# Performance work log

Hardware: AMD Instinct MI355X
Metric: run time of the kernel (lower is better)

## Reference

```python
import jax, jax.numpy as jnp
import numpy as np

G = 4096   # num_genes
P = 4096   # num_perts
H = 64     # hidden_size
B = 4      # num_graphs
E1 = 81920 # coexpress edges
E2 = 81920 # GO edges
FF = 512   # transformer ffn
NH = 2     # attention heads
INTER, LAT = 32, 16  # VAE dims

def _bn(x, g, b, eps=1e-5):
    # BatchNorm1d in training mode: batch stats (biased var)
    m = x.mean(0); v = x.var(0)
    return (x - m) / jnp.sqrt(v + eps) * g + b

def _ln(x, g, b, eps=1e-5):
    m = x.mean(-1, keepdims=True); v = x.var(-1, keepdims=True)
    return (x - m) / jnp.sqrt(v + eps) * g + b

def _mlp2(x, w1, b1, g1, be1, w2, b2, g2, be2):
    # MLP([a,b,c]) builds Linear->BN->ReLU->Linear->BN (trailing ReLU stripped)
    h = jax.nn.relu(_bn(x @ w1.T + b1, g1, be1))
    return _bn(h @ w2.T + b2, g2, be2)

def _sgconv(x, ei, ew, w, b, n):
    # SGConv K=1: gcn_norm (self loops, symmetric norm) then linear
    src = jnp.concatenate([ei[0], jnp.arange(n)])
    dst = jnp.concatenate([ei[1], jnp.arange(n)])
    wgt = jnp.concatenate([ew, jnp.ones((n,), ew.dtype)])
    deg = jax.ops.segment_sum(wgt, dst, num_segments=n)
    dinv = jnp.where(deg > 0, 1.0 / jnp.sqrt(jnp.where(deg > 0, deg, 1.0)), 0.0)
    norm = dinv[dst] * wgt * dinv[src]
    agg = jax.ops.segment_sum(norm[:, None] * x[src], dst, num_segments=n)
    return agg @ w.T + b

def setup_inputs():
    ks = iter(jax.random.split(jax.random.key(0), 80))
    def nrm(shape, s=0.05):
        return jax.random.normal(next(ks), shape, dtype=jnp.float32) * s
    d = {}
    d['x'] = jax.random.uniform(next(ks), (B * G,), dtype=jnp.float32)
    d['pert_idx'] = jax.random.randint(next(ks), (B, 2), 0, P)
    d['mask'] = jnp.zeros((G, G), jnp.float32)
    d['ei_co'] = jax.random.randint(next(ks), (2, E1), 0, G)
    d['w_co'] = jax.random.uniform(next(ks), (E1,), dtype=jnp.float32)
    d['ei_go'] = jax.random.randint(next(ks), (2, E2), 0, P)
    d['w_go'] = jax.random.uniform(next(ks), (E2,), dtype=jnp.float32)
    d['gene_emb'] = nrm((G, H)); d['emb_pos'] = nrm((G, H)); d['pert_tbl'] = nrm((P, H))
    d['sg_co_w'] = nrm((H, H)); d['sg_co_b'] = jnp.zeros((H,))
    d['sg_go_w'] = nrm((H, H)); d['sg_go_b'] = jnp.zeros((H,))
    d['bn_emb_g'] = jnp.ones((H,)); d['bn_emb_b'] = jnp.zeros((H,))
    for pre, din, dout in [('etv2_1', H, H), ('etv2_2', H, H), ('pf_1', H, H), ('pf_2', H, H), ('rw_1', H, 2 * H), ('rw_2', 2 * H, H)]:
        d[pre + '_w'] = nrm((dout, din)); d[pre + '_b'] = jnp.zeros((dout,))
        d[pre + '_g'] = jnp.ones((dout,)); d[pre + '_be'] = jnp.zeros((dout,))
    d['bnpb_g'] = jnp.ones((H,)); d['bnpb_b'] = jnp.zeros((H,))
    d['attn_in_w'] = nrm((3 * H, H)); d['attn_in_b'] = jnp.zeros((3 * H,))
    d['attn_out_w'] = nrm((H, H)); d['attn_out_b'] = jnp.zeros((H,))
    d['ln1_g'] = jnp.ones((H,)); d['ln1_b'] = jnp.zeros((H,))
    d['ff1_w'] = nrm((FF, H)); d['ff1_b'] = jnp.zeros((FF,))
    d['ff2_w'] = nrm((H, FF)); d['ff2_b'] = jnp.zeros((H,))
    d['ln2_g'] = jnp.ones((H,)); d['ln2_b'] = jnp.zeros((H,))
    d['indv_w1'] = nrm((G, H)); d['indv_b1'] = jnp.zeros((G,))
    d['vae_e1_w'] = nrm((INTER, G)); d['vae_e1_b'] = jnp.zeros((INTER,))
    d['vae_mu_w'] = nrm((LAT, INTER)); d['vae_mu_b'] = jnp.zeros((LAT,))
    d['vae_lv_w'] = nrm((LAT, INTER)); d['vae_lv_b'] = jnp.zeros((LAT,))
    d['vae_d1_w'] = nrm((INTER, LAT)); d['vae_d1_b'] = jnp.zeros((INTER,))
    d['vae_d2_w'] = nrm((G, INTER)); d['vae_d2_b'] = jnp.zeros((G,))
    d['eps'] = jax.random.normal(next(ks), (B, LAT), dtype=jnp.float32)
    return d

def reference(x, pert_idx, mask, ei_co, w_co, ei_go, w_go, gene_emb, emb_pos, pert_tbl, sg_co_w, sg_co_b, sg_go_w, sg_go_b, bn_emb_g, bn_emb_b, etv2_1_w, etv2_1_b, etv2_1_g, etv2_1_be, etv2_2_w, etv2_2_b, etv2_2_g, etv2_2_be, pf_1_w, pf_1_b, pf_1_g, pf_1_be, pf_2_w, pf_2_b, pf_2_g, pf_2_be, rw_1_w, rw_1_b, rw_1_g, rw_1_be, rw_2_w, rw_2_b, rw_2_g, rw_2_be, bnpb_g, bnpb_b, attn_in_w, attn_in_b, attn_out_w, attn_out_b, ln1_g, ln1_b, ff1_w, ff1_b, ff2_w, ff2_b, ln2_g, ln2_b, indv_w1, indv_b1, vae_e1_w, vae_e1_b, vae_mu_w, vae_mu_b, vae_lv_w, vae_lv_b, vae_d1_w, vae_d1_b, vae_d2_w, vae_d2_b, eps):
    # gene base embedding (identical across graphs until pert fusion)
    base = jax.nn.relu(_bn(gene_emb, bn_emb_g, bn_emb_b))               # [G,H]
    pos = _sgconv(emb_pos, ei_co, w_co, sg_co_w, sg_co_b, G)            # 1 gene-GNN layer
    base = base + 0.2 * pos
    base = _mlp2(base, etv2_1_w, etv2_1_b, etv2_1_g, etv2_1_be, etv2_2_w, etv2_2_b, etv2_2_g, etv2_2_be)
    # pert embeddings propagated on GO graph
    pge = _sgconv(pert_tbl, ei_go, w_go, sg_go_w, sg_go_b, P)           # [P,H]
    # per-graph pert_track: sum of pert embeddings (all pert_idx valid)
    psum = pge[pert_idx].sum(axis=1)                                    # [B,H]
    etot = _mlp2(psum, pf_1_w, pf_1_b, pf_1_g, pf_1_be, pf_2_w, pf_2_b, pf_2_g, pf_2_be)
    base_b = base[None, :, :] + etot[:, None, :]                        # [B,G,H]
    flat = jax.nn.relu(_bn(base_b.reshape(B * G, H), bnpb_g, bnpb_b))
    out = _mlp2(flat, rw_1_w, rw_1_b, rw_1_g, rw_1_be, rw_2_w, rw_2_b, rw_2_g, rw_2_be)
    out = out.reshape(B, G, H)
    # transformer encoder layer (post-norm, relu, nhead=2), eval/no-dropout
    qkv = out @ attn_in_w.T + attn_in_b
    q, k, v = jnp.split(qkv, 3, axis=-1)
    hd = H // NH
    q = q.reshape(B, G, NH, hd); k = k.reshape(B, G, NH, hd); v = v.reshape(B, G, NH, hd)
    sc = jnp.einsum('bqhd,bkhd->bhqk', q, k) / np.float32(np.sqrt(hd)) + mask
    a = jax.nn.softmax(sc, axis=-1)
    ctx = jnp.einsum('bhqk,bkhd->bqhd', a, v).reshape(B, G, H)
    att = ctx @ attn_out_w.T + attn_out_b
    h1 = _ln(out + att, ln1_g, ln1_b)
    ff = jax.nn.relu(h1 @ ff1_w.T + ff1_b) @ ff2_w.T + ff2_b
    enc = _ln(h1 + ff, ln2_g, ln2_b)
    # per-gene linear: (enc.unsqueeze(-1)*indv_w1).sum(2)+indv_b1
    pred0 = jnp.einsum('bgh,gh->bg', enc, indv_w1) + indv_b1
    # VAE branch on raw expression
    xr = x.reshape(B, G)
    he = jax.nn.relu(xr @ vae_e1_w.T + vae_e1_b)
    mu = he @ vae_mu_w.T + vae_mu_b
    lv = he @ vae_lv_w.T + vae_lv_b
    z = mu + eps * jnp.exp(0.5 * lv)
    hdc = jax.nn.relu(z @ vae_d1_w.T + vae_d1_b)
    recon = hdc @ vae_d2_w.T + vae_d2_b
    kl = -0.5 * jnp.mean(jnp.sum(1.0 + lv - mu ** 2 - jnp.exp(lv), axis=1))
    recon = jnp.where(xr == 0, 0.0, recon)
    pred = pred0 + recon
    return (pred, kl)
```

## Files before the change

### kernel.cpp

```cpp
#include <hip/hip_runtime.h>
#include <hip/hip_bf16.h>
#include <math.h>

#define GG 4096
#define PP 4096
#define HH 64
#define BB 4
#define E1N 81920
#define E2N 81920
#define FFD 512
#define BNEPS 1e-5f
#define LOG2E 1.44269504088896341f
#define QPRE (0.17677669529663687f * LOG2E)

typedef unsigned short ushort_t;
typedef unsigned int uint_t;
using sh8 = __attribute__((ext_vector_type(8))) short;
using sh4 = __attribute__((ext_vector_type(4))) short;
using f4  = __attribute__((ext_vector_type(4))) float;

struct MaskOn  { static constexpr bool v = true; };
struct MaskOff { static constexpr bool v = false; };

#if __has_builtin(__builtin_amdgcn_mfma_f32_16x16x16bf16_1k)
// ... 341 lines not shown
        dev_pert_edges(bid - 320, pidx, ei_go, w_go, ws + OF_DEGGO, pert_tbl, ws + OF_PSLOT);
    else dev_vae_mid(ws + OF_HE, vmu_w, vmu_b, vlv_w, vlv_b, vd1_w, vd1_b, veps,
                     ws + OF_HDC, klout, sh);
}

__global__ void k_fat4(float* ws, const float* __restrict__ gene_emb,
                       const float* __restrict__ emb_pos,
                       const float* __restrict__ sg_co_w, const float* __restrict__ sg_co_b,
                       const float* __restrict__ bn_emb_g, const float* __restrict__ bn_emb_b,
                       const int* __restrict__ pidx, const float* __restrict__ pert_tbl,
                       const float* __restrict__ gw, const float* __restrict__ gb,
                       const float* __restrict__ w1, const float* __restrict__ b1,
                       const float* __restrict__ g1, const float* __restrict__ be1,
                       const float* __restrict__ w2, const float* __restrict__ b2,
                       const float* __restrict__ g2, const float* __restrict__ be2) {
    __shared__ float sh[4416];
    int bid = blockIdx.x;
    if (bid < 1024)
        dev_base_combine(bid, gene_emb, (const int*)(ws + OF_OFFS),
                         (const int*)(ws + OF_SSRC), ws + OF_SNRM,
                         emb_pos, ws + OF_DEGCO,
                         sg_co_w, sg_co_b, ws + OF_STATS, ws + OF_STATS + 128,
                         bn_emb_g, bn_emb_b, ws + OF_BASEIN, sh);
    else
        dev_pert_mlp(ws + OF_PSLOT, pidx, ws + OF_DEGGO, pert_tbl, gw, gb,
                     w1, b1, g1, be1, w2, b2, g2, be2, ws + OF_ETOT, sh);
}

__launch_bounds__(256)
__global__ void k_gemm64(const float* __restrict__ X, const float* __restrict__ W,
                         const float* __restrict__ bias, float* __restrict__ Y,
                         int Cin, int Cout,
                         const float* __restrict__ bnsum, const float* __restrict__ bnsq,
                         const float* __restrict__ bng, const float* __restrict__ bnb,
                         float invN, int relu_in,
                         float* __restrict__ outsum, float* __restrict__ outsq) {
    __shared__ float Xs[64][66];
    __shared__ float Ws[64][66];
    __shared__ float bsc[64], bsh[64];
    const int t = threadIdx.x;
    const int row0 = blockIdx.x * 64, cb = blockIdx.y * 64;
    const int tx = t & 15, ty = t >> 4;
    const int c0 = tx * 4, r0 = ty * 4;
    float acc[4][4];
    #pragma unroll
    for (int j = 0; j < 4; j++)
        #pragma unroll
        for (int i = 0; i < 4; i++) acc[j][i] = 0.f;

    for (int k0 = 0; k0 < Cin; k0 += 64) {
        __syncthreads();
        if (t < 64) {
            float sc = 1.f, sh = 0.f;
            if (bnsum) {
                int c = k0 + t;
                float m = bnsum[c] * invN;
                float is_ = rsqrtf(bnsq[c] * invN - m * m + BNEPS);
                sc = is_ * bng[c]; sh = bnb[c] - m * sc;
            }
            bsc[t] = sc; bsh[t] = sh;
        }
        __syncthreads();
        for (int i = t; i < 1024; i += 256) {
            int r = i >> 4, kq = (i & 15) * 4;
            float4 v = *(const float4*)&X[(size_t)(row0 + r) * Cin + k0 + kq];
            float e0 = v.x * bsc[kq] + bsh[kq];
            float e1 = v.y * bsc[kq + 1] + bsh[kq + 1];
            float e2 = v.z * bsc[kq + 2] + bsh[kq + 2];
            float e3 = v.w * bsc[kq + 3] + bsh[kq + 3];
            if (relu_in) {
                e0 = fmaxf(e0, 0.f); e1 = fmaxf(e1, 0.f);
                e2 = fmaxf(e2, 0.f); e3 = fmaxf(e3, 0.f);
            }
            Xs[r][kq] = e0; Xs[r][kq + 1] = e1; Xs[r][kq + 2] = e2; Xs[r][kq + 3] = e3;
            float4 wv = *(const float4*)&W[(size_t)(cb + r) * Cin + k0 + kq];
            Ws[r][kq] = wv.x; Ws[r][kq + 1] = wv.y; Ws[r][kq + 2] = wv.z; Ws[r][kq + 3] = wv.w;
        }
        __syncthreads();
        #pragma unroll 4
        for (int k = 0; k < 64; k += 2) {
            float2 a[4], b[4];
            #pragma unroll
            for (int j = 0; j < 4; j++) a[j] = *(const float2*)&Xs[r0 + j][k];
            #pragma unroll
            for (int i = 0; i < 4; i++) b[i] = *(const float2*)&Ws[c0 + i][k];
            #pragma unroll
            for (int j = 0; j < 4; j++)
                #pragma unroll
                for (int i = 0; i < 4; i++)
                    acc[j][i] += a[j].x * b[i].x + a[j].y * b[i].y;
        }
    }
    float4 bi = *(const float4*)&bias[cb + c0];
    float scol[4] = {0.f, 0.f, 0.f, 0.f}, qcol[4] = {0.f, 0.f, 0.f, 0.f};
    #pragma unroll
    for (int j = 0; j < 4; j++) {
        float4 o;
        o.x = acc[j][0] + bi.x; o.y = acc[j][1] + bi.y;
        o.z = acc[j][2] + bi.z; o.w = acc[j][3] + bi.w;
        *(float4*)&Y[(size_t)(row0 + r0 + j) * Cout + cb + c0] = o;
        scol[0] += o.x; scol[1] += o.y; scol[2] += o.z; scol[3] += o.w;
        qcol[0] += o.x * o.x; qcol[1] += o.y * o.y;
        qcol[2] += o.z * o.z; qcol[3] += o.w * o.w;
    }
    if (outsum) {
        __syncthreads();
        #pragma unroll
        for (int i = 0; i < 4; i++) { Xs[ty][c0 + i] = scol[i]; Ws[ty][c0 + i] = qcol[i]; }
        __syncthreads();
        if (t < 64) {
            float ss = 0.f, qq = 0.f;
            #pragma unroll
            for (int r = 0; r < 16; r++) { ss += Xs[r][t]; qq += Ws[r][t]; }
            atomicAdd(&outsum[cb + t], ss);
            atomicAdd(&outsq[cb + t], qq);
        }
    }
}

__launch_bounds__(256)
__global__ void k_gemm_rw1(const float* __restrict__ y2, const float* __restrict__ etot,
                           const float* __restrict__ s2sum, const float* __restrict__ s2sq,
                           const float* __restrict__ g2e, const float* __restrict__ b2e,
                           const float* __restrict__ g3, const float* __restrict__ b3,
                           const float* __restrict__ W, const float* __restrict__ bias,
                           float* __restrict__ Y,
                           float* __restrict__ osum, float* __restrict__ osq) {
    __shared__ float Xs[64][66];
    __shared__ float Ws[64][66];
    __shared__ float bsc[64], bsh[64];
    const int t = threadIdx.x;
    const int row0 = blockIdx.x * 64, cb = blockIdx.y * 64;
    const int tx = t & 15, ty = t >> 4;
    const int c0 = tx * 4, r0 = ty * 4;
    const int bb = row0 >> 12;
    if (t < 64) {
        const float iG = 1.0f / 4096.f, iNG = 1.0f / 16384.f;
        float S1 = s2sum[t], S2 = s2sq[t];
        float m2 = S1 * iG;
        float is2 = rsqrtf(S2 * iG - m2 * m2 + BNEPS);
        float sc2 = is2 * g2e[t], sh2 = b2e[t] - m2 * sc2;
        float sz = sc2 * S1 + 4096.f * sh2;
        float szz = sc2 * sc2 * S2 + 2.f * sc2 * sh2 * S1 + 4096.f * sh2 * sh2;
        float e0 = etot[t], e1 = etot[64 + t], e2 = etot[128 + t], e3 = etot[192 + t];
        float se = e0 + e1 + e2 + e3;
        float see = e0 * e0 + e1 * e1 + e2 * e2 + e3 * e3;
        float sumF = 4.f * sz + 4096.f * se;
        float sqF = 4.f * szz + 2.f * sz * se + 4096.f * see;
        float m3 = sumF * iNG;
        float is3 = rsqrtf(sqF * iNG - m3 * m3 + BNEPS);
        float eb = etot[bb * 64 + t];
        bsc[t] = sc2 * is3 * g3[t];
        bsh[t] = (sh2 + eb - m3) * is3 * g3[t] + b3[t];
    }
    __syncthreads();
    for (int i = t; i < 1024; i += 256) {
        int r = i >> 4, kq = (i & 15) * 4;
        int g = (row0 + r) & 4095;
        float4 v = *(const float4*)&y2[(size_t)g * 64 + kq];
        Xs[r][kq] = fmaxf(v.x * bsc[kq] + bsh[kq], 0.f);
        Xs[r][kq + 1] = fmaxf(v.y * bsc[kq + 1] + bsh[kq + 1], 0.f);
        Xs[r][kq + 2] = fmaxf(v.z * bsc[kq + 2] + bsh[kq + 2], 0.f);
        Xs[r][kq + 3] = fmaxf(v.w * bsc[kq + 3] + bsh[kq + 3], 0.f);
        float4 wv = *(const float4*)&W[(size_t)(cb + r) * 64 + kq];
        Ws[r][kq] = wv.x; Ws[r][kq + 1] = wv.y; Ws[r][kq + 2] = wv.z; Ws[r][kq + 3] = wv.w;
    }
    __syncthreads();
    float acc[4][4];
    #pragma unroll
    for (int j = 0; j < 4; j++)
        #pragma unroll
        for (int i = 0; i < 4; i++) acc[j][i] = 0.f;
    #pragma unroll 4
    for (int k = 0; k < 64; k += 2) {
        float2 a[4], b[4];
        #pragma unroll
        for (int j = 0; j < 4; j++) a[j] = *(const float2*)&Xs[r0 + j][k];
        #pragma unroll
        for (int i = 0; i < 4; i++) b[i] = *(const float2*)&Ws[c0 + i][k];
        #pragma unroll
        for (int j = 0; j < 4; j++)
            #pragma unroll
            for (int i = 0; i < 4; i++)
                acc[j][i] += a[j].x * b[i].x + a[j].y * b[i].y;
    }
    float4 bi = *(const float4*)&bias[cb + c0];
    float scol[4] = {0.f, 0.f, 0.f, 0.f}, qcol[4] = {0.f, 0.f, 0.f, 0.f};
    #pragma unroll
    for (int j = 0; j < 4; j++) {
        float4 o;
        o.x = acc[j][0] + bi.x; o.y = acc[j][1] + bi.y;
        o.z = acc[j][2] + bi.z; o.w = acc[j][3] + bi.w;
        *(float4*)&Y[(size_t)(row0 + r0 + j) * 128 + cb + c0] = o;
        scol[0] += o.x; scol[1] += o.y; scol[2] += o.z; scol[3] += o.w;
        qcol[0] += o.x * o.x; qcol[1] += o.y * o.y;
        qcol[2] += o.z * o.z; qcol[3] += o.w * o.w;
    }
    __syncthreads();
    #pragma unroll
    for (int i = 0; i < 4; i++) { Xs[ty][c0 + i] = scol[i]; Ws[ty][c0 + i] = qcol[i]; }
    __syncthreads();
    if (t < 64) {
        float ss = 0.f, qq = 0.f;
        #pragma unroll
        for (int r = 0; r < 16; r++) { ss += Xs[r][t]; qq += Ws[r][t]; }
        atomicAdd(&osum[cb + t], ss);
        atomicAdd(&osq[cb + t], qq);
    }
}

__launch_bounds__(256)
__global__ void k_gemm_qkv(const float* __restrict__ X, const float* __restrict__ W,
                           const float* __restrict__ bias,
                           const float* __restrict__ bnsum, const float* __restrict__ bnsq,
                           const float* __restrict__ bng, const float* __restrict__ bnb,
                           ushort_t* __restrict__ Qb, ushort_t* __restrict__ Kb,
                           ushort_t* __restrict__ Vf) {
    __shared__ float Xs[64][66];
    __shared__ float Ws[64][66];
    __shared__ float bsc[64], bsh[64];
    const int t = threadIdx.x;
    const int row0 = blockIdx.x * 64, yb = blockIdx.y, cb = yb * 64;
    const int tx = t & 15, ty = t >> 4;
    const int c0 = tx * 4, r0 = ty * 4;
    const float invN = 1.0f / (float)(BB * GG);
    if (t < 64) {
        float m = bnsum[t] * invN;
        float is_ = rsqrtf(bnsq[t] * invN - m * m + BNEPS);
        float sc = is_ * bng[t];
        bsc[t] = sc; bsh[t] = bnb[t] - m * sc;
    }
    __syncthreads();
    for (int i = t; i < 1024; i += 256) {
        int r = i >> 4, kq = (i & 15) * 4;
        float4 v = *(const float4*)&X[(size_t)(row0 + r) * 64 + kq];
        Xs[r][kq] = v.x * bsc[kq] + bsh[kq];
        Xs[r][kq + 1] = v.y * bsc[kq + 1] + bsh[kq + 1];
        Xs[r][kq + 2] = v.z * bsc[kq + 2] + bsh[kq + 2];
        Xs[r][kq + 3] = v.w * bsc[kq + 3] + bsh[kq + 3];
        float4 wv = *(const float4*)&W[(size_t)(cb + r) * 64 + kq];
        Ws[r][kq] = wv.x; Ws[r][kq + 1] = wv.y; Ws[r][kq + 2] = wv.z; Ws[r][kq + 3] = wv.w;
    }
    __syncthreads();
    float acc[4][4];
    #pragma unroll
    for (int j = 0; j < 4; j++)
        #pragma unroll
        for (int i = 0; i < 4; i++) acc[j][i] = 0.f;
    #pragma unroll 4
    for (int k = 0; k < 64; k += 2) {
        float2 a[4], b[4];
        #pragma unroll
        for (int j = 0; j < 4; j++) a[j] = *(const float2*)&Xs[r0 + j][k];
        #pragma unroll
        for (int i = 0; i < 4; i++) b[i] = *(const float2*)&Ws[c0 + i][k];
        #pragma unroll
        for (int j = 0; j < 4; j++)
            #pragma unroll
            for (int i = 0; i < 4; i++)
                acc[j][i] += a[j].x * b[i].x + a[j].y * b[i].y;
    }
    float4 bi = *(const float4*)&bias[cb + c0];
    const int b2 = row0 >> 12, tile = (row0 & 4095) >> 6;
    if (yb < 2) {
        ushort_t* Dst = (yb == 0) ? Qb : Kb;
        const float sc2 = (yb == 0) ? QPRE : 1.0f;
        const int h = c0 >> 5, d = c0 & 31;
        #pragma unroll
        for (int j = 0; j < 4; j++) {
            union { ushort_t u[4]; uint2 v; } pk;
            pk.u[0] = f2b((acc[j][0] + bi.x) * sc2);
            pk.u[1] = f2b((acc[j][1] + bi.y) * sc2);
            pk.u[2] = f2b((acc[j][2] + bi.z) * sc2);
            pk.u[3] = f2b((acc[j][3] + bi.w) * sc2);
            int g = (row0 & 4095) + r0 + j;
            *(uint2*)&Dst[((size_t)(b2 * 2 + h) * GG + g) * 32 + d] = pk.v;
        }
    } else {
        __syncthreads();
        #pragma unroll
        for (int j = 0; j < 4; j++) {
            Xs[r0 + j][c0] = acc[j][0] + bi.x;
            Xs[r0 + j][c0 + 1] = acc[j][1] + bi.y;
            Xs[r0 + j][c0 + 2] = acc[j][2] + bi.z;
            Xs[r0 + j][c0 + 3] = acc[j][3] + bi.w;
        }
        __syncthreads();
        #pragma unroll
        for (int h = 0; h < 2; h++) {
            union { ushort_t u[8]; uint4 v; } pk;
            #pragma unroll
            for (int j = 0; j < 8; j++) {
                int idx = t * 8 + j;
                int g2 = idx >> 8, L = (idx >> 2) & 63, i = idx & 3;
                int key = (g2 >> 1) * 16 + ((L >> 4) << 2) + i;
                int d = ((g2 & 1) << 4) + (L & 15);
                pk.u[j] = f2b(Xs[key][h * 32 + d]);
            }
            *(uint4*)&Vf[((size_t)((b2 * 2 + h) * 64 + tile)) * 2048 + t * 8] = pk.v;
        }
    }
}

__launch_bounds__(512, 8)
__global__ void k_attn_mfma(const ushort_t* __restrict__ Qb, const ushort_t* __restrict__ Kb,
                            const ushort_t* __restrict__ Vf, const float* __restrict__ mask,
                            const float* __restrict__ mflag,
                            float* __restrict__ opA, float* __restrict__ opB,
                            float* __restrict__ Lp) {
    __shared__ ushort_t Kl[2][2][2048];
    __shared__ ushort_t Vl[2][2][2048];
    const int split = blockIdx.y;
    const int bh0 = blockIdx.z * 2;
    const int q0 = blockIdx.x * 64;
    const int kstart = split * (GG / 4), kend = kstart + (GG / 4);
    const int t = threadIdx.x;
    const int lane = t & 63, w = t >> 6;
    const int qg = w >> 1, kh = w & 1;
    const int l15 = lane & 15, quad = lane >> 4;
    const int i2a = kh * 2, i2b = kh * 2 + 1;
    const int um = (*(const int*)mflag) != 0;

    sh8 qf[2];
    #pragma unroll
    for (int bh = 0; bh < 2; bh++)
        qf[bh] = *(const sh8*)&Qb[((size_t)(bh0 + bh) * GG + q0 + qg * 16 + l15) * 32 + quad * 8];
    const float* mrow = mask + (size_t)(q0 + qg * 16 + l15) * GG + quad * 4;

    auto stage = [&](int buf, int k0) {
        int bh = t >> 8, c = t & 255;
        int key = ((c >> 6) << 4) + (c & 15);
        int chunk = (c >> 4) & 3;
        gld16(Kb + ((size_t)(bh0 + bh) * GG + k0 + key) * 32 + chunk * 8,
              &Kl[buf][bh][c * 8]);
        gld16(Vf + ((size_t)((bh0 + bh) * 64 + (k0 >> 6))) * 2048 + c * 8,
              &Vl[buf][bh][c * 8]);
    };
    stage(0, kstart);

    f4 O0[2], O1[2];
    float ls[2];
    #pragma unroll
    for (int bh = 0; bh < 2; bh++) {
        O0[bh] = f4{0.f, 0.f, 0.f, 0.f};
        O1[bh] = f4{0.f, 0.f, 0.f, 0.f};
        ls[bh] = 0.f;
    }

    auto run = [&](auto tag) {
        constexpr bool U = decltype(tag)::v;
        const float4 zf4 = {0.f, 0.f, 0.f, 0.f};
        float4 mva = zf4, mvb = zf4;
        if constexpr (U) {
            mva = *(const float4*)&mrow[kstart + i2a * 16];
            mvb = *(const float4*)&mrow[kstart + i2b * 16];
        }
        for (int k0 = kstart; k0 < kend; k0 += 64) {
            const int cur = ((k0 - kstart) >> 6) & 1;
            __syncthreads();
            if (k0 + 64 < kend) stage(cur ^ 1, k0 + 64);
            float4 mva_n = zf4, mvb_n = zf4;
            if constexpr (U) {
                const int kp = (k0 + 64 < kend) ? (k0 + 64) : k0;
                mva_n = *(const float4*)&mrow[kp + i2a * 16];
                mvb_n = *(const float4*)&mrow[kp + i2b * 16];
            }
            #pragma unroll
            for (int bh = 0; bh < 2; bh++) {
                sh8 kfa = *(const sh8*)&Kl[cur][bh][(i2a * 64 + lane) * 8];
                sh8 kfb = *(const sh8*)&Kl[cur][bh][(i2b * 64 + lane) * 8];
                f4 z = {0.f, 0.f, 0.f, 0.f};
                f4 sa = __builtin_amdgcn_mfma_f32_16x16x32_bf16(kfa, qf[bh], z, 0, 0, 0);
                f4 sb = __builtin_amdgcn_mfma_f32_16x16x32_bf16(kfb, qf[bh], z, 0, 0, 0);
                {
                    float p0, p1, p2, p3;
                    if constexpr (U) {
                        p0 = exp2f(fmaf(mva.x, LOG2E, sa[0]));
                        p1 = exp2f(fmaf(mva.y, LOG2E, sa[1]));
                        p2 = exp2f(fmaf(mva.z, LOG2E, sa[2]));
                        p3 = exp2f(fmaf(mva.w, LOG2E, sa[3]));
                    } else {
                        p0 = exp2f(sa[0]); p1 = exp2f(sa[1]);
                        p2 = exp2f(sa[2]); p3 = exp2f(sa[3]);
                    }
                    ls[bh] += (p0 + p1) + (p2 + p3);
                    union { __hip_bfloat162 h2[2]; sh4 v; } pkp;
                    pkp.h2[0] = __float22bfloat162_rn(float2{p0, p1});
                    pkp.h2[1] = __float22bfloat162_rn(float2{p2, p3});
                    sh4 vf0 = *(const sh4*)&Vl[cur][bh][((i2a * 2 + 0) * 64 + lane) * 4];
                    sh4 vf1 = *(const sh4*)&Vl[cur][bh][((i2a * 2 + 1) * 64 + lane) * 4];
                    O0[bh] = MFMA16(pkp.v, vf0, O0[bh]);
                    O1[bh] = MFMA16(pkp.v, vf1, O1[bh]);
                }
                {
                    float p0, p1, p2, p3;
                    if constexpr (U) {
                        p0 = exp2f(fmaf(mvb.x, LOG2E, sb[0]));
                        p1 = exp2f(fmaf(mvb.y, LOG2E, sb[1]));
                        p2 = exp2f(fmaf(mvb.z, LOG2E, sb[2]));
                        p3 = exp2f(fmaf(mvb.w, LOG2E, sb[3]));
                    } else {
                        p0 = exp2f(sb[0]); p1 = exp2f(sb[1]);
                        p2 = exp2f(sb[2]); p3 = exp2f(sb[3]);
                    }
                    ls[bh] += (p0 + p1) + (p2 + p3);
                    union { __hip_bfloat162 h2[2]; sh4 v; } pkp;
                    pkp.h2[0] = __float22bfloat162_rn(float2{p0, p1});
                    pkp.h2[1] = __float22bfloat162_rn(float2{p2, p3});
                    sh4 vf0 = *(const sh4*)&Vl[cur][bh][((i2b * 2 + 0) * 64 + lane) * 4];
                    sh4 vf1 = *(const sh4*)&Vl[cur][bh][((i2b * 2 + 1) * 64 + lane) * 4];
                    O0[bh] = MFMA16(pkp.v, vf0, O0[bh]);
                    O1[bh] = MFMA16(pkp.v, vf1, O1[bh]);
                }
            }
            if constexpr (U) { mva = mva_n; mvb = mvb_n; }
        }
    };
    if (um) run(MaskOn{}); else run(MaskOff{});

    #pragma unroll
    for (int bh = 0; bh < 2; bh++) {
        ls[bh] += __shfl_xor(ls[bh], 16, 64);
        ls[bh] += __shfl_xor(ls[bh], 32, 64);
    }
    __syncthreads();
    float* Ox = (float*)&Kl[0][0][0];
    float* Lx = (float*)&Vl[0][0][0];
    if (kh == 0) {
        #pragma unroll
        for (int bh = 0; bh < 2; bh++) {
            #pragma unroll
            for (int r = 0; r < 4; r++) {
                int ql = qg * 16 + quad * 4 + r;
                Ox[(bh * 64 + ql) * 32 + l15] = O0[bh][r];
                Ox[(bh * 64 + ql) * 32 + l15 + 16] = O1[bh][r];
            }
            if (quad == 0) Lx[bh * 64 + qg * 16 + l15] = ls[bh];
        }
    }
    __syncthreads();
    if (kh == 1) {
        float* op = (split < 3) ? (opA + (size_t)split * OPS) : opB;
        #pragma unroll
        for (int bh = 0; bh < 2; bh++) {
            int gbh = bh0 + bh;
            #pragma unroll
            for (int r = 0; r < 4; r++) {
                int ql = qg * 16 + quad * 4 + r;
                size_t o = ((size_t)gbh * GG + q0 + ql) * 32 + l15;
                op[o] = O0[bh][r] + Ox[(bh * 64 + ql) * 32 + l15];
                op[o + 16] = O1[bh][r] + Ox[(bh * 64 + ql) * 32 + l15 + 16];
            }
            if (quad == 0)
                Lp[split * 32768 + gbh * GG + q0 + qg * 16 + l15] =
                    ls[bh] + Lx[bh * 64 + qg * 16 + l15];
        }
    }
}

__launch_bounds__(256)
__global__ void k_tail(const float* __restrict__ opA, const float* __restrict__ opB,
                       const float* __restrict__ Lp, const float* __restrict__ yrw2,
                       const float* __restrict__ Waout, const float* __restrict__ baout,
                       const float* __restrict__ bsum5, const float* __restrict__ bsq5,
                       const float* __restrict__ bg5, const float* __restrict__ bb5,
                       const float* __restrict__ lg1, const float* __restrict__ lb1,
                       const ushort_t* __restrict__ W1b, const float* __restrict__ b1f,
                       const ushort_t* __restrict__ W2b, const float* __restrict__ b2f,
                       const float* __restrict__ lg2, const float* __restrict__ lb2,
                       const float* __restrict__ indvw, const float* __restrict__ indvb,
                       const float* __restrict__ hdc, const float* __restrict__ d2w,
                       const float* __restrict__ d2b, const float* __restrict__ x,
                       float* __restrict__ outp) {
    __shared__ float Wt[4160];
    __shared__ float Cs[4160];
    __shared__ ushort_t Hb[4096];
    __shared__ ushort_t FT[32768];
    __shared__ ushort_t WS[2][4096];
    const int t = threadIdx.x;
    const int r0b = blockIdx.x * 64;
    const int lane = t & 63, w = t >> 6;
    const int l15 = lane & 15, quad = lane >> 4;

    for (int i = t; i < 4096; i += 256) Wt[(i & 63) * 65 + (i >> 6)] = Waout[i];
    {
        int col = t & 63, rl = t >> 6;
        int hh = col >> 5, d = col & 31;
        for (int jj = 0; jj < 16; jj++) {
            int lrow = rl + jj * 4;
            int row = r0b + lrow;
            int b = row >> 12, q = row & 4095;
            int bhq = (b * 2 + hh) * GG + q;
            size_t oi = (size_t)bhq * 32 + d;
            float num = opA[oi] + opA[OPS + oi] + opA[2 * OPS + oi] + opB[oi];
            float den = Lp[bhq] + Lp[32768 + bhq] + Lp[65536 + bhq] + Lp[98304 + bhq];
            Cs[lrow * 65 + col] = num / den;
        }
    }
    __syncthreads();
    const float invN = 1.0f / (float)(BB * GG);
    float m5 = bsum5[lane] * invN;
    float is5 = rsqrtf(bsq5[lane] * invN - m5 * m5 + BNEPS);
    float h1v[16];
    for (int j = 0; j < 16; j++) {
        int lrow = w * 16 + j;
        int row = r0b + lrow;
        float acc = baout[lane];
        const float* cr = Cs + lrow * 65;
        #pragma unroll 8
        for (int k = 0; k < 64; k++) acc += cr[k] * Wt[k * 65 + lane];
        float ov = (yrw2[(size_t)row * 64 + lane] - m5) * is5 * bg5[lane] + bb5[lane];
        float v = ov + acc;
        float s = v;
        for (int o = 32; o > 0; o >>= 1) s += __shfl_xor(s, o, 64);
        float mean = s * (1.f / 64.f);
        float d = v - mean;
        float sq = d * d;
        for (int o = 32; o > 0; o >>= 1) sq += __shfl_xor(sq, o, 64);
        float inv = rsqrtf(sq * (1.f / 64.f) + BNEPS);
        h1v[j] = d * inv * lg1[lane] + lb1[lane];
    }
    __syncthreads();
    float* h1f = Wt;
    for (int j = 0; j < 16; j++) h1f[(w * 16 + j) * 65 + lane] = h1v[j];
    __syncthreads();
    if (t < 128) {
        int kt = t >> 6, lane6 = t & 63;
        int q2 = (lane6 >> 4) & 3, r15 = lane6 & 15;
        for (int rg = 0; rg < 4; rg++) {
            union { ushort_t u[8]; uint4 v4; } pk;
            #pragma unroll
            for (int j = 0; j < 8; j++)
                pk.u[j] = f2b(h1f[(rg * 16 + r15) * 65 + kt * 32 + q2 * 8 + j]);
            *(uint4*)&Hb[(rg * 2 + kt) * 512 + lane6 * 8] = pk.v4;
        }
    }
    auto stage1 = [&](int buf, int cb8) {
        int cb = cb8 * 64;
        #pragma unroll
        for (int kt = 0; kt < 2; kt++)
            gld16(W1b + (size_t)((cb + w * 16 + l15) * 64 + kt * 32 + quad * 8),
                  &WS[buf][(w * 2 + kt) * 512 + lane * 8]);
    };
    stage1(0, 0);
    for (int cb8 = 0; cb8 < 8; cb8++) {
        const int cur = cb8 & 1;
        __syncthreads();
        if (cb8 + 1 < 8) stage1(cur ^ 1, cb8 + 1);
        sh8 xf0 = *(const sh8*)&Hb[(w * 2 + 0) * 512 + lane * 8];
        sh8 xf1 = *(const sh8*)&Hb[(w * 2 + 1) * 512 + lane * 8];
        const int cb = cb8 * 64;
        #pragma unroll
        for (int c = 0; c < 4; c++) {
            sh8 wf0 = *(const sh8*)&WS[cur][(c * 2 + 0) * 512 + lane * 8];
            sh8 wf1 = *(const sh8*)&WS[cur][(c * 2 + 1) * 512 + lane * 8];
            f4 z = {0.f, 0.f, 0.f, 0.f};
            f4 acc = __builtin_amdgcn_mfma_f32_16x16x32_bf16(wf0, xf0, z, 0, 0, 0);
            acc = __builtin_amdgcn_mfma_f32_16x16x32_bf16(wf1, xf1, acc, 0, 0, 0);
            float4 bv = *(const float4*)&b1f[cb + c * 16 + quad * 4];
            union { ushort_t u[4]; uint2 v2; } pk;
            pk.u[0] = f2b(fmaxf(acc[0] + bv.x, 0.f));
            pk.u[1] = f2b(fmaxf(acc[1] + bv.y, 0.f));
            pk.u[2] = f2b(fmaxf(acc[2] + bv.z, 0.f));
            pk.u[3] = f2b(fmaxf(acc[3] + bv.w, 0.f));
            int kt512 = cb8 * 2 + (c >> 1);
            int quadp = (c & 1) * 2 + (quad >> 1);
            int j0 = (quad & 1) * 4;
            *(uint2*)&FT[((w * 16 + kt512) * 64 + quadp * 16 + l15) * 8 + j0] = pk.v2;
        }
    }
    auto stage2 = [&](int buf, int k0) {
        #pragma unroll
        for (int kt = 0; kt < 2; kt++)
            gld16(W2b + (size_t)((w * 16 + l15) * 512 + k0 + kt * 32 + quad * 8),
                  &WS[buf][(w * 2 + kt) * 512 + lane * 8]);
    };
    stage2(0, 0);
    f4 acc2[4];
    #pragma unroll
    for (int c = 0; c < 4; c++) acc2[c] = f4{0.f, 0.f, 0.f, 0.f};
    for (int k0 = 0; k0 < 512; k0 += 64) {
        const int cur = (k0 >> 6) & 1;
        __syncthreads();
        if (k0 + 64 < 512) stage2(cur ^ 1, k0 + 64);
        const int ktb = k0 >> 5;
        #pragma unroll
        for (int kt = 0; kt < 2; kt++) {
            sh8 xf = *(const sh8*)&FT[((w * 16 + ktb + kt) * 64 + lane) * 8];
            #pragma unroll
            for (int c = 0; c < 4; c++) {
                sh8 wf = *(const sh8*)&WS[cur][(c * 2 + kt) * 512 + lane * 8];
                acc2[c] = __builtin_amdgcn_mfma_f32_16x16x32_bf16(wf, xf, acc2[c], 0, 0, 0);
            }
        }
    }
    const int row = r0b + w * 16 + l15;
    const int b = row >> 12, g = row & 4095;
    float v[4][4];
    float s = 0.f, sq = 0.f;
    #pragma unroll
    for (int c = 0; c < 4; c++) {
        float4 bv = *(const float4*)&b2f[c * 16 + quad * 4];
        #pragma unroll
        for (int i = 0; i < 4; i++) {
            float hv = h1f[(w * 16 + l15) * 65 + c * 16 + quad * 4 + i];
            float bvi = (i == 0) ? bv.x : (i == 1) ? bv.y : (i == 2) ? bv.z : bv.w;
            v[c][i] = hv + acc2[c][i] + bvi;
            s += v[c][i]; sq += v[c][i] * v[c][i];
        }
    }
    s += __shfl_xor(s, 16, 64);  s += __shfl_xor(s, 32, 64);
    sq += __shfl_xor(sq, 16, 64); sq += __shfl_xor(sq, 32, 64);
    float mean = s * (1.f / 64.f);
    float inv = rsqrtf(sq * (1.f / 64.f) - mean * mean + BNEPS);
    float pd = 0.f;
    #pragma unroll
    for (int c = 0; c < 4; c++) {
        float4 lgv = *(const float4*)&lg2[c * 16 + quad * 4];
        float4 lbv = *(const float4*)&lb2[c * 16 + quad * 4];
        float4 iwv = *(const float4*)&indvw[(size_t)g * 64 + c * 16 + quad * 4];
        pd += ((v[c][0] - mean) * inv * lgv.x + lbv.x) * iwv.x;
        pd += ((v[c][1] - mean) * inv * lgv.y + lbv.y) * iwv.y;
        pd += ((v[c][2] - mean) * inv * lgv.z + lbv.z) * iwv.z;
        pd += ((v[c][3] - mean) * inv * lgv.w + lbv.w) * iwv.w;
    }
    float rc = 0.f;
    #pragma unroll
    for (int i = 0; i < 8; i++)
        rc += hdc[b * 32 + quad * 8 + i] * d2w[(size_t)g * 32 + quad * 8 + i];
    pd += __shfl_xor(pd, 16, 64); pd += __shfl_xor(pd, 32, 64);
    rc += __shfl_xor(rc, 16, 64); rc += __shfl_xor(rc, 32, 64);
    if (quad == 0) {
        float recon = rc + d2b[g];
        if (x[row] == 0.f) recon = 0.f;
        outp[row] = pd + indvb[g] + recon;
    }
}

extern "C" void kernel_launch(void* const* d_in, const int* in_sizes, int n_in,
                              void* d_out, int out_size, void* d_ws, size_t ws_size,
                              hipStream_t stream) {
    const float* x        = (const float*)d_in[0];
    const int*   pert_idx = (const int*)  d_in[1];
    const float* mask     = (const float*)d_in[2];
    const int*   ei_co    = (const int*)  d_in[3];
    const float* w_co     = (const float*)d_in[4];
    const int*   ei_go    = (const int*)  d_in[5];
    const float* w_go     = (const float*)d_in[6];
    const float* gene_emb = (const float*)d_in[7];
    const float* emb_pos  = (const float*)d_in[8];
    const float* pert_tbl = (const float*)d_in[9];
    const float* sg_co_w  = (const float*)d_in[10];
    const float* sg_co_b  = (const float*)d_in[11];
    const float* sg_go_w  = (const float*)d_in[12];
    const float* sg_go_b  = (const float*)d_in[13];
    const float* bn_emb_g = (const float*)d_in[14];
    const float* bn_emb_b = (const float*)d_in[15];
    const float* etv1_w   = (const float*)d_in[16];
    const float* etv1_b   = (const float*)d_in[17];
    const float* etv1_g   = (const float*)d_in[18];
    const float* etv1_be  = (const float*)d_in[19];
    const float* etv2_w   = (const float*)d_in[20];
    const float* etv2_b   = (const float*)d_in[21];
    const float* etv2_g   = (const float*)d_in[22];
    const float* etv2_be  = (const float*)d_in[23];
    const float* pf1_w    = (const float*)d_in[24];
    const float* pf1_b    = (const float*)d_in[25];
    const float* pf1_g    = (const float*)d_in[26];
    const float* pf1_be   = (const float*)d_in[27];
    const float* pf2_w    = (const float*)d_in[28];
    const float* pf2_b    = (const float*)d_in[29];
    const float* pf2_g    = (const float*)d_in[30];
    const float* pf2_be   = (const float*)d_in[31];
    const float* rw1_w    = (const float*)d_in[32];
    const float* rw1_b    = (const float*)d_in[33];
    const float* rw1_g    = (const float*)d_in[34];
    const float* rw1_be   = (const float*)d_in[35];
    const float* rw2_w    = (const float*)d_in[36];
    const float* rw2_b    = (const float*)d_in[37];
    const float* rw2_g    = (const float*)d_in[38];
    const float* rw2_be   = (const float*)d_in[39];
    const float* bnpb_g   = (const float*)d_in[40];
    const float* bnpb_b   = (const float*)d_in[41];
    const float* ain_w    = (const float*)d_in[42];
    const float* ain_b    = (const float*)d_in[43];
    const float* aout_w   = (const float*)d_in[44];
    const float* aout_b   = (const float*)d_in[45];
    const float* ln1_g    = (const float*)d_in[46];
    const float* ln1_b    = (const float*)d_in[47];
    const float* ff1_w    = (const float*)d_in[48];
    const float* ff1_b    = (const float*)d_in[49];
    const float* ff2_w    = (const float*)d_in[50];
    const float* ff2_b    = (const float*)d_in[51];
    const float* ln2_g    = (const float*)d_in[52];
    const float* ln2_b    = (const float*)d_in[53];
    const float* indv_w   = (const float*)d_in[54];
    const float* indv_b   = (const float*)d_in[55];
    const float* ve1_w    = (const float*)d_in[56];
    const float* ve1_b    = (const float*)d_in[57];
    const float* vmu_w    = (const float*)d_in[58];
    const float* vmu_b    = (const float*)d_in[59];
    const float* vlv_w    = (const float*)d_in[60];
    const float* vlv_b    = (const float*)d_in[61];
    const float* vd1_w    = (const float*)d_in[62];
    const float* vd1_b    = (const float*)d_in[63];
    const float* vd2_w    = (const float*)d_in[64];
    const float* vd2_b    = (const float*)d_in[65];
    const float* veps     = (const float*)d_in[66];

    float* ws   = (float*)d_ws;
    float* outp = (float*)d_out;

    float* stm1 = ws + OF_STATS + 1 * 256; float* sti1 = stm1 + 128;
    float* stm2 = ws + OF_STATS + 2 * 256; float* sti2 = stm2 + 128;
    float* stm4 = ws + OF_STATS + 4 * 256; float* sti4 = stm4 + 128;
    float* stm5 = ws + OF_STATS + 5 * 256; float* sti5 = stm5 + 128;

    float* basein = ws + OF_BASEIN;
    float* y1     = ws + OF_Y1;
    float* y2     = ws + OF_Y2;
    float* yrw1   = ws + OF_RW1;
    float* yrw2   = ws + OF_RW2;
    float* opA    = ws + OF_OPA;
    float* opB    = ws + OF_OPB;
    float* Lp     = ws + OF_LP;
    ushort_t* Qb  = (ushort_t*)(ws + OF_QB);
    ushort_t* Kb  = (ushort_t*)(ws + OF_KB);
    ushort_t* Vf  = (ushort_t*)(ws + OF_VF);
    ushort_t* W1b = (ushort_t*)(ws + OF_W1B);
    ushort_t* W2b = (ushort_t*)(ws + OF_W2B);

    const int NG = BB * GG;
    const float iG = 1.0f / (float)GG, iNG = 1.0f / (float)NG;

    hipMemsetAsync(ws, 0, 11268 * sizeof(float), stream);
    hipMemsetAsync(ws + OF_CNT, 0, 4096 * sizeof(int), stream);

    k_fat12<<<1792, 256, 0, stream>>>(ws, ei_co, w_co, ei_go, w_go, gene_emb,
                                      x, ve1_w, ve1_b, ff1_w, ff2_w, mask);
    k_scan<<<1, 256, 0, stream>>>(ws);
    k_fat3<<<641, 256, 0, stream>>>(ws, ei_co, w_co, pert_idx,
                                    ei_go, w_go, pert_tbl,
                                    vmu_w, vmu_b, vlv_w, vlv_b, vd1_w, vd1_b,
                                    veps, outp + NG);
    k_fat4<<<1025, 256, 0, stream>>>(ws, gene_emb, emb_pos, sg_co_w, sg_co_b,
                                     bn_emb_g, bn_emb_b, pert_idx, pert_tbl,
                                     sg_go_w, sg_go_b,
                                     pf1_w, pf1_b, pf1_g, pf1_be,
                                     pf2_w, pf2_b, pf2_g, pf2_be);
    k_gemm64<<<dim3(GG / 64, 1), 256, 0, stream>>>(basein, etv1_w, etv1_b, y1, 64, 64,
                                                   nullptr, nullptr, nullptr, nullptr, 0.f, 0,
                                                   stm1, sti1);
    k_gemm64<<<dim3(GG / 64, 1), 256, 0, stream>>>(y1, etv2_w, etv2_b, y2, 64, 64,
                                                   stm1, sti1, etv1_g, etv1_be, iG, 1,
                                                   stm2, sti2);
    k_gemm_rw1<<<dim3(NG / 64, 2), 256, 0, stream>>>(y2, ws + OF_ETOT, stm2, sti2,
                                                     etv2_g, etv2_be, bnpb_g, bnpb_b,
                                                     rw1_w, rw1_b, yrw1, stm4, sti4);
    k_gemm64<<<dim3(NG / 64, 1), 256, 0, stream>>>(yrw1, rw2_w, rw2_b, yrw2, 128, 64,
                                                   stm4, sti4, rw1_g, rw1_be, iNG, 1,
                                                   stm5, sti5);
    k_gemm_qkv<<<dim3(NG / 64, 3), 256, 0, stream>>>(yrw2, ain_w, ain_b,
                                                     stm5, sti5, rw2_g, rw2_be,
                                                     Qb, Kb, Vf);
    k_attn_mfma<<<dim3(GG / 64, 4, 4), 512, 0, stream>>>(Qb, Kb, Vf, mask,
                                                         ws + OF_MFLAG, opA, opB, Lp);
    k_tail<<<NG / 64, 256, 0, stream>>>(opA, opB, Lp, yrw2, aout_w, aout_b,
                                        stm5, sti5, rw2_g, rw2_be, ln1_g, ln1_b,
                                        W1b, ff1_b, W2b, ff2_b, ln2_g, ln2_b,
                                        indv_w, indv_b, ws + OF_HDC, vd2_w, vd2_b,
                                        x, outp);
}
```

Before: 455.4 us.

## Halve attention key splits and double key tile per iteration

The attention kernel now splits the key range two ways instead of four, and each iteration stages and processes 128 keys instead of 64. Shared memory K/V buffers double and the launch bound drops to 4 blocks per CU. The split-combine in the tail kernel reads only two partial outputs and normalisers. The aim is to cut partial-sum traffic and the number of barriers per key. The cost is fewer blocks in flight (512 instead of 1024), lower occupancy, and mask loads that are no longer prefetched one iteration ahead.

```diff
diff --git a/kernel.cpp b/kernel.cpp
--- a/kernel.cpp
+++ b/kernel.cpp
@@ -667,23 +667,22 @@
     }
 }
 
-__launch_bounds__(512, 8)
+__launch_bounds__(512, 4)
 __global__ void k_attn_mfma(const ushort_t* __restrict__ Qb, const ushort_t* __restrict__ Kb,
                             const ushort_t* __restrict__ Vf, const float* __restrict__ mask,
                             const float* __restrict__ mflag,
                             float* __restrict__ opA, float* __restrict__ opB,
                             float* __restrict__ Lp) {
-    __shared__ ushort_t Kl[2][2][2048];
-    __shared__ ushort_t Vl[2][2][2048];
+    __shared__ ushort_t Kl[2][2][4096];
+    __shared__ ushort_t Vl[2][2][4096];
     const int split = blockIdx.y;
     const int bh0 = blockIdx.z * 2;
     const int q0 = blockIdx.x * 64;
-    const int kstart = split * (GG / 4), kend = kstart + (GG / 4);
+    const int kstart = split * (GG / 2), kend = kstart + (GG / 2);
     const int t = threadIdx.x;
     const int lane = t & 63, w = t >> 6;
     const int qg = w >> 1, kh = w & 1;
     const int l15 = lane & 15, quad = lane >> 4;
-    const int i2a = kh * 2, i2b = kh * 2 + 1;
     const int um = (*(const int*)mflag) != 0;
 
     sh8 qf[2];
@@ -696,10 +695,13 @@
         int bh = t >> 8, c = t & 255;
         int key = ((c >> 6) << 4) + (c & 15);
         int chunk = (c >> 4) & 3;
-        gld16(Kb + ((size_t)(bh0 + bh) * GG + k0 + key) * 32 + chunk * 8,
-              &Kl[buf][bh][c * 8]);
-        gld16(Vf + ((size_t)((bh0 + bh) * 64 + (k0 >> 6))) * 2048 + c * 8,
-              &Vl[buf][bh][c * 8]);
+        #pragma unroll
+        for (int s = 0; s < 2; s++) {
+            gld16(Kb + ((size_t)(bh0 + bh) * GG + k0 + s * 64 + key) * 32 + chunk * 8,
+                  &Kl[buf][bh][s * 2048 + c * 8]);
+            gld16(Vf + ((size_t)((bh0 + bh) * 64 + (k0 >> 6) + s)) * 2048 + c * 8,
+                  &Vl[buf][bh][s * 2048 + c * 8]);
+        }
     };
     stage(0, kstart);
 
@@ -714,36 +716,25 @@
 
     auto run = [&](auto tag) {
         constexpr bool U = decltype(tag)::v;
-        const float4 zf4 = {0.f, 0.f, 0.f, 0.f};
-        float4 mva = zf4, mvb = zf4;
-        if constexpr (U) {
-            mva = *(const float4*)&mrow[kstart + i2a * 16];
-            mvb = *(const float4*)&mrow[kstart + i2b * 16];
-        }
-        for (int k0 = kstart; k0 < kend; k0 += 64) {
-            const int cur = ((k0 - kstart) >> 6) & 1;
+        for (int k0 = kstart; k0 < kend; k0 += 128) {
+            const int cur = ((k0 - kstart) >> 7) & 1;
             __syncthreads();
-            if (k0 + 64 < kend) stage(cur ^ 1, k0 + 64);
-            float4 mva_n = zf4, mvb_n = zf4;
-            if constexpr (U) {
-                const int kp = (k0 + 64 < kend) ? (k0 + 64) : k0;
-                mva_n = *(const float4*)&mrow[kp + i2a * 16];
-                mvb_n = *(const float4*)&mrow[kp + i2b * 16];
-            }
+            if (k0 + 128 < kend) stage(cur ^ 1, k0 + 128);
             #pragma unroll
             for (int bh = 0; bh < 2; bh++) {
-                sh8 kfa = *(const sh8*)&Kl[cur][bh][(i2a * 64 + lane) * 8];
-                sh8 kfb = *(const sh8*)&Kl[cur][bh][(i2b * 64 + lane) * 8];
-                f4 z = {0.f, 0.f, 0.f, 0.f};
-                f4 sa = __builtin_amdgcn_mfma_f32_16x16x32_bf16(kfa, qf[bh], z, 0, 0, 0);
-                f4 sb = __builtin_amdgcn_mfma_f32_16x16x32_bf16(kfb, qf[bh], z, 0, 0, 0);
-                {
+                #pragma unroll
+                for (int ii = 0; ii < 4; ii++) {
+                    const int i2 = kh * 4 + ii;
+                    sh8 kf = *(const sh8*)&Kl[cur][bh][(i2 * 64 + lane) * 8];
+                    f4 z = {0.f, 0.f, 0.f, 0.f};
+                    f4 sa = __builtin_amdgcn_mfma_f32_16x16x32_bf16(kf, qf[bh], z, 0, 0, 0);
                     float p0, p1, p2, p3;
                     if constexpr (U) {
-                        p0 = exp2f(fmaf(mva.x, LOG2E, sa[0]));
-                        p1 = exp2f(fmaf(mva.y, LOG2E, sa[1]));
-                        p2 = exp2f(fmaf(mva.z, LOG2E, sa[2]));
-                        p3 = exp2f(fmaf(mva.w, LOG2E, sa[3]));
+                        float4 mv = *(const float4*)&mrow[k0 + i2 * 16];
+                        p0 = exp2f(fmaf(mv.x, LOG2E, sa[0]));
+                        p1 = exp2f(fmaf(mv.y, LOG2E, sa[1]));
+                        p2 = exp2f(fmaf(mv.z, LOG2E, sa[2]));
+                        p3 = exp2f(fmaf(mv.w, LOG2E, sa[3]));
                     } else {
                         p0 = exp2f(sa[0]); p1 = exp2f(sa[1]);
                         p2 = exp2f(sa[2]); p3 = exp2f(sa[3]);
@@ -752,33 +743,12 @@
                     union { __hip_bfloat162 h2[2]; sh4 v; } pkp;
                     pkp.h2[0] = __float22bfloat162_rn(float2{p0, p1});
                     pkp.h2[1] = __float22bfloat162_rn(float2{p2, p3});
-                    sh4 vf0 = *(const sh4*)&Vl[cur][bh][((i2a * 2 + 0) * 64 + lane) * 4];
-                    sh4 vf1 = *(const sh4*)&Vl[cur][bh][((i2a * 2 + 1) * 64 + lane) * 4];
-                    O0[bh] = MFMA16(pkp.v, vf0, O0[bh]);
-                    O1[bh] = MFMA16(pkp.v, vf1, O1[bh]);
-                }
-                {
-                    float p0, p1, p2, p3;
-                    if constexpr (U) {
-                        p0 = exp2f(fmaf(mvb.x, LOG2E, sb[0]));
-                        p1 = exp2f(fmaf(mvb.y, LOG2E, sb[1]));
-                        p2 = exp2f(fmaf(mvb.z, LOG2E, sb[2]));
-                        p3 = exp2f(fmaf(mvb.w, LOG2E, sb[3]));
-                    } else {
-                        p0 = exp2f(sb[0]); p1 = exp2f(sb[1]);
-                        p2 = exp2f(sb[2]); p3 = exp2f(sb[3]);
-                    }
-                    ls[bh] += (p0 + p1) + (p2 + p3);
-                    union { __hip_bfloat162 h2[2]; sh4 v; } pkp;
-                    pkp.h2[0] = __float22bfloat162_rn(float2{p0, p1});
-                    pkp.h2[1] = __float22bfloat162_rn(float2{p2, p3});
-                    sh4 vf0 = *(const sh4*)&Vl[cur][bh][((i2b * 2 + 0) * 64 + lane) * 4];
-                    sh4 vf1 = *(const sh4*)&Vl[cur][bh][((i2b * 2 + 1) * 64 + lane) * 4];
+                    sh4 vf0 = *(const sh4*)&Vl[cur][bh][((i2 * 2 + 0) * 64 + lane) * 4];
+                    sh4 vf1 = *(const sh4*)&Vl[cur][bh][((i2 * 2 + 1) * 64 + lane) * 4];
                     O0[bh] = MFMA16(pkp.v, vf0, O0[bh]);
                     O1[bh] = MFMA16(pkp.v, vf1, O1[bh]);
                 }
             }
-            if constexpr (U) { mva = mva_n; mvb = mvb_n; }
         }
     };
     if (um) run(MaskOn{}); else run(MaskOff{});
@@ -805,7 +775,7 @@
     }
     __syncthreads();
     if (kh == 1) {
-        float* op = (split < 3) ? (opA + (size_t)split * OPS) : opB;
+        float* op = (split == 0) ? opA : opB;
         #pragma unroll
         for (int bh = 0; bh < 2; bh++) {
             int gbh = bh0 + bh;
@@ -857,8 +827,8 @@
             int b = row >> 12, q = row & 4095;
             int bhq = (b * 2 + hh) * GG + q;
             size_t oi = (size_t)bhq * 32 + d;
-            float num = opA[oi] + opA[OPS + oi] + opA[2 * OPS + oi] + opB[oi];
-            float den = Lp[bhq] + Lp[32768 + bhq] + Lp[65536 + bhq] + Lp[98304 + bhq];
+            float num = opA[oi] + opB[oi];
+            float den = Lp[bhq] + Lp[32768 + bhq];
             Cs[lrow * 65 + col] = num / den;
         }
     }
@@ -1128,7 +1098,7 @@
     k_gemm_qkv<<<dim3(NG / 64, 3), 256, 0, stream>>>(yrw2, ain_w, ain_b,
                                                      stm5, sti5, rw2_g, rw2_be,
                                                      Qb, Kb, Vf);
-    k_attn_mfma<<<dim3(GG / 64, 4, 4), 512, 0, stream>>>(Qb, Kb, Vf, mask,
+    k_attn_mfma<<<dim3(GG / 64, 2, 4), 512, 0, stream>>>(Qb, Kb, Vf, mask,
                                                          ws + OF_MFLAG, opA, opB, Lp);
     k_tail<<<NG / 64, 256, 0, stream>>>(opA, opB, Lp, yrw2, aout_w, aout_b,
                                         stm5, sti5, rw2_g, rw2_be, ln1_g, ln1_b,
```

New measurement: 445.7 us. 1.02x faster.
